# Performance work log

Measured on AMD Instinct MI355X. Metric: run time of the kernel, lower is better.

## Reference

```python
import jax, jax.numpy as jnp
import numpy as np

G = 4          # moe_groups
EPG = 4        # experts per group = e_num // moe_groups
E = 16         # e_num
KG = 2         # moe_max_groups
K = 2          # moe_max_k
GTP = 0.9      # moe_group_top_p
TP = 0.9       # moe_top_p
SCALE = 1.0 / float(np.sqrt(G))  # group_scale


def setup_inputs() -> dict:
    key = jax.random.key(0)
    ks = jax.random.split(key, 6)
    B, T, D, H = 2, 1024, 512, 2048  # H = 4*emb_dim per SwiGLU_FFN(emb_dim, 4*emb_dim)
    x = jax.random.normal(ks[0], (B, T, D), jnp.float32)
    Wr = jax.random.normal(ks[1], (D, G), jnp.float32) * 0.02      # group_router weight
    br = jnp.zeros((G,), jnp.float32)                               # group_router bias
    Wgate = jax.random.normal(ks[2], (G, D, EPG), jnp.float32) * 0.02  # per-group gates
    bgate = jnp.zeros((G, EPG), jnp.float32)
    W1 = jax.random.normal(ks[3], (E, D, H), jnp.float32) * 0.02   # SwiGLU gate proj
    W3 = jax.random.normal(ks[4], (E, D, H), jnp.float32) * 0.02   # SwiGLU up proj
    W2 = jax.random.normal(ks[5], (E, H, D), jnp.float32) * 0.02   # SwiGLU down proj
    return {"x": x, "Wr": Wr, "br": br, "Wgate": Wgate, "bgate": bgate,
            "W1": W1, "W3": W3, "W2": W2}


def _routing_weights(xf, Wr, br, Wgate, bgate):
    # Returns combined per-(token, expert) weight (N, E): group_renorm * expert_renorm * SCALE.
    N = xf.shape[0]
    # ---- group-level top-p routing ----
    gp = jax.nn.softmax(xf @ Wr + br, axis=-1)                      # (N, G)
    order = jnp.argsort(-gp, axis=-1)
    sp_k = jnp.take_along_axis(gp, order, axis=-1)[:, :KG]          # top-KG probs, descending
    idx_k = order[:, :KG]
    act = jnp.cumsum(sp_k, axis=-1) <= GTP
    act = act.at[:, 0].set(True)                                    # always keep best group
    mp = sp_k * act
    rn = mp / (jnp.sum(mp, axis=-1, keepdims=True) + 1e-9)
    w_group = jnp.zeros((N, G), xf.dtype).at[jnp.arange(N)[:, None], idx_k].set(rn)
    # ---- expert-level top-p routing within each group ----
    ep = jax.nn.softmax(jnp.einsum('nd,gde->nge', xf, Wgate) + bgate, axis=-1)  # (N, G, EPG)
    eorder = jnp.argsort(-ep, axis=-1)
    esp = jnp.take_along_axis(ep, eorder, axis=-1)[:, :, :K]
    eidx = eorder[:, :, :K]
    eact = jnp.cumsum(esp, axis=-1) <= TP
    eact = eact.at[:, :, 0].set(True)                               # always keep best expert
    emp = esp * eact
    ern = emp / (jnp.sum(emp, axis=-1, keepdims=True) + 1e-9)
    w_exp = jnp.zeros((N, G, EPG), xf.dtype).at[
        jnp.arange(N)[:, None, None], jnp.arange(G)[None, :, None], eidx].set(ern)
    return (w_group[:, :, None] * w_exp * SCALE).reshape(N, E)      # (N, E)


def reference(x, Wr, br, Wgate, bgate, W1, W3, W2):
    B, T, D = x.shape
    xf = x.reshape(-1, D)                                           # (N, D)
    tw = _routing_weights(xf, Wr, br, Wgate, bgate)                 # (N, E)
    out = jnp.zeros_like(xf)
    for e in range(E):  # fixed structural loop over experts
        h = jax.nn.silu(xf @ W1[e]) * (xf @ W3[e])                  # SwiGLU hidden (N, H)
        out = out + tw[:, e:e + 1] * (h @ W2[e])
    return out.reshape(B, T, D)
```

## Files before the change

### kernel.cpp

```cpp
#include <hip/hip_runtime.h>
#include <math.h>

typedef unsigned short u16;
typedef unsigned int   u32;
typedef short s16x8 __attribute__((ext_vector_type(8)));
typedef float f32x4 __attribute__((ext_vector_type(4)));

#define N_TOK 2048
#define DIM   512
#define HID   2048
#define NE    16
#define NG    4
#define EPG   4
#define MAXT  2048

#define BM 64
#define BN 128
#define BK 64

#define WS_CNT    0
#define WS_OFF    128
#define WS_TOKIDX 256
#define WS_TW     (WS_TOKIDX + NE*MAXT*4)
#define WS_XB     (WS_TW + N_TOK*NE*4)
#define WS_HBUF   (WS_XB + (size_t)N_TOK*DIM*2)
#define WS_W1T    (WS_HBUF + (size_t)8192*HID*2)
#define WS_W3T    (WS_W1T + (size_t)NE*HID*DIM*2)
#define WS_W2T    (WS_W3T + (size_t)NE*HID*DIM*2)
#define WS_SLOT   (WS_W2T + (size_t)NE*DIM*HID*2)
#define WS_BUF2   WS_W1T

__device__ __forceinline__ int* ws_i32(void* ws, size_t off) { return (int*)((char*)ws + off); }

__device__ __forceinline__ u16 f2b(float f) {
    union { float f; u32 i; } v; v.f = f;
    u32 b = v.i;
    u32 r = b + 0x7FFFu + ((b >> 16) & 1u);
    return (u16)(r >> 16);
}

__device__ __forceinline__ void gl_lds16(const u16* g, u16* l) {
    __builtin_amdgcn_global_load_lds((const __attribute__((address_space(1))) void*)g,
                                     (__attribute__((address_space(3))) void*)l, 16, 0, 0);
}

__global__ __launch_bounds__(1024) void prep_kernel(
    const float* __restrict__ x, const float* __restrict__ Wr, const float* __restrict__ br,
    const float* __restrict__ Wgate, const float* __restrict__ bgate,
    const float* __restrict__ W1, const float* __restrict__ W3, void* ws)
{
    __shared__ u16 T[2][128*128];
    int tid = threadIdx.x;
    int bid = blockIdx.x;

    if (bid < 128) {
        int t = bid * 16 + (tid >> 6);
        int lane = tid & 63;

        float xl[8];
        {
            const float4* xr = (const float4*)(x + (size_t)t*DIM + lane*8);
            float4 a = xr[0], b = xr[1];
            xl[0]=a.x; xl[1]=a.y; xl[2]=a.z; xl[3]=a.w;
            xl[4]=b.x; xl[5]=b.y; xl[6]=b.z; xl[7]=b.w;
        }
        {
            union { u16 h[8]; uint4 q; } pk;
            #pragma unroll
            for (int i = 0; i < 8; i++) pk.h[i] = f2b(xl[i]);
            u16* xb = (u16*)((char*)ws + WS_XB);
            *(uint4*)(xb + (size_t)t*DIM + lane*8) = pk.q;
        }

        float gl[NG] = {0.f,0.f,0.f,0.f};
        float el[NE];
        #pragma unroll
        for (int e = 0; e < NE; e++) el[e] = 0.f;

        {
            const float4* Wr4 = (const float4*)Wr;
            #pragma unroll
            for (int c = 0; c < 8; c++) {
                float4 w = Wr4[lane*8 + c];
                gl[0] += xl[c]*w.x; gl[1] += xl[c]*w.y;
                gl[2] += xl[c]*w.z; gl[3] += xl[c]*w.w;
            }
        }
        {
            const float4* Wg4 = (const float4*)Wgate;
            #pragma unroll
            for (int g = 0; g < NG; g++) {
                #pragma unroll
                for (int c = 0; c < 8; c++) {
                    float4 w = Wg4[(size_t)g*DIM + lane*8 + c];
                    el[g*4+0] += xl[c]*w.x; el[g*4+1] += xl[c]*w.y;
                    el[g*4+2] += xl[c]*w.z; el[g*4+3] += xl[c]*w.w;
                }
            }
        }

        #pragma unroll
        for (int g = 0; g < NG; g++)
            #pragma unroll
            for (int s = 32; s; s >>= 1) gl[g] += __shfl_xor(gl[g], s);
        #pragma unroll
        for (int e = 0; e < NE; e++)
            #pragma unroll
            for (int s = 32; s; s >>= 1) el[e] += __shfl_xor(el[e], s);

        if (lane != 0) return;

        float gp[NG];
        float mx = -1e30f;
        #pragma unroll
        for (int g = 0; g < NG; g++) { gl[g] += br[g]; mx = fmaxf(mx, gl[g]); }
        float sum = 0.f;
        #pragma unroll
        for (int g = 0; g < NG; g++) { gp[g] = expf(gl[g] - mx); sum += gp[g]; }
        #pragma unroll
        for (int g = 0; g < NG; g++) gp[g] /= sum;

        int i0 = 0;
        #pragma unroll
        for (int g = 1; g < NG; g++) if (gp[g] > gp[i0]) i0 = g;
        int i1 = -1;
        #pragma unroll
        for (int g = 0; g < NG; g++) { if (g == i0) continue; if (i1 < 0 || gp[g] > gp[i1]) i1 = g; }

        bool act1 = (gp[i0] + gp[i1]) <= 0.9f;
        float mp0 = gp[i0], mp1 = act1 ? gp[i1] : 0.f;
        float inv = 1.f / (mp0 + mp1 + 1e-9f);
        float wg[NG] = {0.f,0.f,0.f,0.f};
        wg[i0] = mp0 * inv;
        wg[i1] = mp1 * inv;

        float tw[NE];
        #pragma unroll
        for (int g = 0; g < NG; g++) {
            float ep[EPG];
            float emx = -1e30f;
            #pragma unroll
            for (int j = 0; j < EPG; j++) {
                float v = el[g*4 + j] + bgate[g*4 + j];
                ep[j] = v; emx = fmaxf(emx, v);
            }
            float es = 0.f;
            #pragma unroll
            for (int j = 0; j < EPG; j++) { ep[j] = expf(ep[j] - emx); es += ep[j]; }
            #pragma unroll
            for (int j = 0; j < EPG; j++) ep[j] /= es;

            int j0 = 0;
            #pragma unroll
            for (int j = 1; j < EPG; j++) if (ep[j] > ep[j0]) j0 = j;
            int j1 = -1;
            #pragma unroll
            for (int j = 0; j < EPG; j++) { if (j == j0) continue; if (j1 < 0 || ep[j] > ep[j1]) j1 = j; }

            bool ea1 = (ep[j0] + ep[j1]) <= 0.9f;
            float e0 = ep[j0], e1 = ea1 ? ep[j1] : 0.f;
            float einv = 1.f / (e0 + e1 + 1e-9f);
            float we[EPG] = {0.f,0.f,0.f,0.f};
            we[j0] = e0 * einv;
            we[j1] = e1 * einv;
            #pragma unroll
            for (int j = 0; j < EPG; j++) tw[g*4 + j] = wg[g] * we[j] * 0.5f;
        }

        float* twT = (float*)((char*)ws + WS_TW);
        #pragma unroll
        for (int e = 0; e < NE; e++) twT[(size_t)e*N_TOK + t] = tw[e];
        return;
    }

    int bx = bid - 128;
    int j = tid & 31, i0 = tid >> 5;
    int tg0 = bx * 4;

    const float* src; u16* dst; int k0, n0;
    float4 v0, v1, v2, v3;

    auto setup = [&](int tg) {
        int mat = tg >> 10, e = (tg >> 6) & 15, w = tg & 63;
        const float* s  = mat ? W3 : W1;
        u16* d = (u16*)((char*)ws + (mat ? WS_W3T : WS_W1T));
        k0 = (w & 3) << 7; n0 = (w >> 2) << 7;
        src = s + (size_t)e*DIM*HID + (size_t)(k0 + 4*i0)*HID + n0 + 4*j;
        dst = d + (size_t)e*HID*DIM;
    };
    auto issue_loads = [&]() {
        v0 = *(const float4*)(src);
        v1 = *(const float4*)(src + HID);
        v2 = *(const float4*)(src + 2*HID);
        v3 = *(const float4*)(src + 3*HID);
    };

    setup(tg0);
    issue_loads();

    for (int it = 0; it < 4; ++it) {
        u16* dstc = dst; int k0c = k0, n0c = n0;
        u16* Tb = &T[it & 1][0];

        int pc = 4 * (i0 ^ ((j & 15) << 1));
        union { u16 h[4]; uint2 q; } p;
        p.h[0]=f2b(v0.x); p.h[1]=f2b(v1.x); p.h[2]=f2b(v2.x); p.h[3]=f2b(v3.x);
        *(uint2*)(&Tb[(4*j+0)*128 + pc]) = p.q;
        p.h[0]=f2b(v0.y); p.h[1]=f2b(v1.y); p.h[2]=f2b(v2.y); p.h[3]=f2b(v3.y);
        *(uint2*)(&Tb[(4*j+1)*128 + pc]) = p.q;
        p.h[0]=f2b(v0.z); p.h[1]=f2b(v1.z); p.h[2]=f2b(v2.z); p.h[3]=f2b(v3.z);
        *(uint2*)(&Tb[(4*j+2)*128 + pc]) = p.q;
        p.h[0]=f2b(v0.w); p.h[1]=f2b(v1.w); p.h[2]=f2b(v2.w); p.h[3]=f2b(v3.w);
        *(uint2*)(&Tb[(4*j+3)*128 + pc]) = p.q;

        if (it + 1 < 4) { setup(tg0 + it + 1); issue_loads(); }

        asm volatile("s_waitcnt lgkmcnt(0)" ::: "memory");
        __builtin_amdgcn_s_barrier();

        #pragma unroll
        for (int ph = 0; ph < 2; ++ph) {
            int idx = tid + ph*1024;
            int nr = idx >> 4, sg = idx & 15;
            int cp = (2*sg) ^ (((nr >> 2) & 15) << 1);
            *(s16x8*)(dstc + (size_t)(n0c+nr)*DIM + k0c + sg*8) = *(const s16x8*)(&Tb[nr*128 + 4*cp]);
        }
    }
}

__global__ __launch_bounds__(1024) void expert_scan_kernel(void* ws)
{
    int tid = threadIdx.x;
    int e = tid >> 6, lane = tid & 63;
    const float* twT = (const float*)((char*)ws + WS_TW) + (size_t)e*N_TOK;
    int* tok = ws_i32(ws, WS_TOKIDX) + e*MAXT;
    __shared__ int scnt[NE];
    __shared__ int soff[NE+1];

    float v[32];
    #pragma unroll
    for (int r = 0; r < 32; r++) v[r] = twT[r*64 + lane];

    unsigned long long lanemask = (1ull << lane) - 1ull;
    int base = 0;
    #pragma unroll
    for (int r = 0; r < 32; r++) {
        bool a = v[r] > 0.f;
        unsigned long long m = __ballot(a);
        if (a) tok[base + __popcll(m & lanemask)] = r*64 + lane;
        base += __popcll(m);
    }
    if (lane == 0) scnt[e] = base;
    __syncthreads();
    if (tid == 0) {
        int* cnt = ws_i32(ws, WS_CNT);
        int* off = ws_i32(ws, WS_OFF);
        int s = 0;
        for (int i = 0; i < NE; i++) { cnt[i] = scnt[i]; off[i] = s; soff[i] = s; s += scnt[i]; }
        off[NE] = s; soff[NE] = s;
    }
    __syncthreads();

    int* slot_of = ws_i32(ws, WS_SLOT) + e*N_TOK;
    int base2 = soff[e];
    #pragma unroll
    for (int r = 0; r < 32; r++) {
        bool a = v[r] > 0.f;
        unsigned long long m = __ballot(a);
        int pre = __popcll(m & lanemask);
        slot_of[r*64 + lane] = a ? (base2 + pre) : -1;
        base2 += __popcll(m);
    }
}

__global__ __launch_bounds__(256) void gemm1_fast(const float* __restrict__ W2, void* ws)
{
    __shared__ __align__(16) u16 SM[40960];
    int z = blockIdx.z;
    int tid = threadIdx.x;

    if (z == NE) {
        u16* T2 = SM;
        u16* W2T = (u16*)((char*)ws + WS_W2T);
        int slot = blockIdx.x + 16*blockIdx.y;
        int j = tid & 31, i = tid >> 5;
        #pragma unroll 1
        for (int tt = 0; tt < 2; ++tt) {
            int tile = slot + tt*512;
            int e = tile >> 6, w = tile & 63;
            int k0 = (w & 15) << 7, n0 = (w >> 4) << 7;
            const float* s = W2 + (size_t)e*HID*DIM + (size_t)k0*DIM + n0 + 4*j;
            if (tt) __syncthreads();
            #pragma unroll
            for (int c = 0; c < 4; ++c) {
                int kb = 4*i + 32*c;
                const float* base = s + (size_t)kb*DIM;
                float4 v0 = *(const float4*)(base);
                float4 v1 = *(const float4*)(base + DIM);
                float4 v2 = *(const float4*)(base + 2*DIM);
                float4 v3 = *(const float4*)(base + 3*DIM);
                int pc = 4 * ((i + 8*c) ^ ((j & 15) << 1));
                union { u16 h[4]; uint2 q; } p;
                p.h[0]=f2b(v0.x); p.h[1]=f2b(v1.x); p.h[2]=f2b(v2.x); p.h[3]=f2b(v3.x);
                *(uint2*)(&T2[(4*j+0)*128 + pc]) = p.q;
                p.h[0]=f2b(v0.y); p.h[1]=f2b(v1.y); p.h[2]=f2b(v2.y); p.h[3]=f2b(v3.y);
                *(uint2*)(&T2[(4*j+1)*128 + pc]) = p.q;
                p.h[0]=f2b(v0.z); p.h[1]=f2b(v1.z); p.h[2]=f2b(v2.z); p.h[3]=f2b(v3.z);
                *(uint2*)(&T2[(4*j+2)*128 + pc]) = p.q;
                p.h[0]=f2b(v0.w); p.h[1]=f2b(v1.w); p.h[2]=f2b(v2.w); p.h[3]=f2b(v3.w);
                *(uint2*)(&T2[(4*j+3)*128 + pc]) = p.q;
            }
            __syncthreads();
            u16* d = W2T + (size_t)e*DIM*HID;
            #pragma unroll
            for (int ph = 0; ph < 8; ++ph) {
                int idx = tid + ph*256;
                int nr = idx >> 4, sg = idx & 15;
                int cp = (2*sg) ^ (((nr >> 2) & 15) << 1);
                *(s16x8*)(d + (size_t)(n0+nr)*HID + k0 + sg*8) = *(const s16x8*)(&T2[nr*128 + 4*cp]);
            }
        }
        return;
    }

    int e  = z;
    const int* cnt = ws_i32(ws, WS_CNT);
    int ce = cnt[e];
    int m0 = blockIdx.y * BM;
    if (m0 >= ce) return;
    int n0 = blockIdx.x * BN;

    const int* off = ws_i32(ws, WS_OFF);
    const int* tok = ws_i32(ws, WS_TOKIDX) + e*MAXT;
    const u16* xb  = (const u16*)((char*)ws + WS_XB);
    const u16* W1T = (const u16*)((char*)ws + WS_W1T) + (size_t)e*HID*DIM;
    const u16* W3T = (const u16*)((char*)ws + WS_W3T) + (size_t)e*HID*DIM;
    u16* hbuf = (u16*)((char*)ws + WS_HBUF);
    int obase = off[e] + m0;

    int wave = tid >> 6, lane = tid & 63;
    int quad = lane >> 4, l16 = lane & 15;
    int swz  = l16 & 7;
    int r8 = lane >> 3, sg = lane & 7;
    int swk = ((sg ^ r8) << 3);

    int m_a0 = m0 + wave*16 + r8;     if (m_a0 >= ce) m_a0 = ce - 1;
    int m_a1 = m0 + wave*16 + 8 + r8; if (m_a1 >= ce) m_a1 = ce - 1;
    const u16* arow0 = xb + (size_t)tok[m_a0]*DIM + swk;
    const u16* arow1 = xb + (size_t)tok[m_a1]*DIM + swk;
    const u16* b1row[4]; const u16* b3row[4];
    #pragma unroll
    for (int i = 0; i < 4; i++) {
        size_t nr = (size_t)(n0 + wave*32 + i*8 + r8)*DIM + swk;
        b1row[i] = W1T + nr;
        b3row[i] = W3T + nr;
    }

    f32x4 acc1[4][2], acc3[4][2];
    #pragma unroll
    for (int mt = 0; mt < 4; mt++)
        #pragma unroll
        for (int nt = 0; nt < 2; nt++) {
            acc1[mt][nt] = (f32x4){0.f,0.f,0.f,0.f};
            acc3[mt][nt] = (f32x4){0.f,0.f,0.f,0.f};
        }

    auto stage = [&](u16* B, int k0) {
        gl_lds16(arow0 + k0, B + (wave*16)*BK);
        gl_lds16(arow1 + k0, B + (wave*16 + 8)*BK);
        #pragma unroll
        for (int i = 0; i < 4; i++) {
            gl_lds16(b1row[i] + k0, B + 4096 + (wave*32 + i*8)*BK);
            gl_lds16(b3row[i] + k0, B + 12288 + (wave*32 + i*8)*BK);
        }
    };
    auto compute = [&](const u16* B) {
        #pragma unroll
        for (int kk = 0; kk < BK; kk += 32) {
            int jj = (kk >> 3) + quad;
            int so = ((jj ^ swz) << 3);
            s16x8 af[4];
            #pragma unroll
            for (int mt = 0; mt < 4; mt++)
                af[mt] = *(const s16x8*)(B + (mt*16 + l16)*BK + so);
            #pragma unroll
            for (int nt = 0; nt < 2; nt++) {
                int n = wave*32 + nt*16 + l16;
                s16x8 b1 = *(const s16x8*)(B + 4096 + n*BK + so);
                s16x8 b3 = *(const s16x8*)(B + 12288 + n*BK + so);
                #pragma unroll
                for (int mt = 0; mt < 4; mt++) {
                    acc1[mt][nt] = __builtin_amdgcn_mfma_f32_16x16x32_bf16(af[mt], b1, acc1[mt][nt], 0, 0, 0);
                    acc3[mt][nt] = __builtin_amdgcn_mfma_f32_16x16x32_bf16(af[mt], b3, acc3[mt][nt], 0, 0, 0);
                }
            }
        }
    };

    u16* SM0 = SM;
    u16* SM1 = SM + 20480;

    stage(SM0, 0);
    #pragma unroll 1
    for (int kt2 = 0; kt2 < 3; ++kt2) {
        int kb = kt2*2*BK;
        stage(SM1, kb + BK);
        asm volatile("s_waitcnt vmcnt(10)" ::: "memory");
        __builtin_amdgcn_s_barrier();
        compute(SM0);
        __builtin_amdgcn_s_barrier();
        stage(SM0, kb + 2*BK);
        asm volatile("s_waitcnt vmcnt(10)" ::: "memory");
        __builtin_amdgcn_s_barrier();
        compute(SM1);
        __builtin_amdgcn_s_barrier();
    }
    stage(SM1, 7*BK);
    asm volatile("s_waitcnt vmcnt(10)" ::: "memory");
    __builtin_amdgcn_s_barrier();
    compute(SM0);
    __builtin_amdgcn_s_barrier();
    asm volatile("s_waitcnt vmcnt(0)" ::: "memory");
    __builtin_amdgcn_s_barrier();
    compute(SM1);

    #pragma unroll
    for (int mt = 0; mt < 4; mt++) {
        #pragma unroll
        for (int r = 0; r < 4; r++) {
            int row = mt*16 + quad*4 + r;
            if (m0 + row < ce) {
                #pragma unroll
                for (int nt = 0; nt < 2; nt++) {
                    float a = acc1[mt][nt][r];
                    float b = acc3[mt][nt][r];
                    float h = (a / (1.f + expf(-a))) * b;
                    int col = wave*32 + nt*16 + l16;
                    hbuf[(size_t)(obase + row)*HID + n0 + col] = f2b(h);
                }
            }
        }
    }
}

__global__ __launch_bounds__(256) void gemm2_fast(void* ws)
{
    __shared__ __align__(16) u16 SM[24576];
    int e  = blockIdx.z;
    const int* cnt = ws_i32(ws, WS_CNT);
    int ce = cnt[e];
    int m0 = blockIdx.y * BM;
    if (m0 >= ce) return;
    int n0 = blockIdx.x * BN;

    const int* off = ws_i32(ws, WS_OFF);
    const int* tok = ws_i32(ws, WS_TOKIDX) + e*MAXT;
    const float* twT = (const float*)((char*)ws + WS_TW);
    const u16* hbuf = (const u16*)((char*)ws + WS_HBUF);
    const u16* W2T = (const u16*)((char*)ws + WS_W2T) + (size_t)e*DIM*HID;
    float* buf2 = (float*)((char*)ws + WS_BUF2);
    int abase = off[e] + m0;
    int total = off[NE];

    int tid = threadIdx.x;
    int wave = tid >> 6, lane = tid & 63;
    int quad = lane >> 4, l16 = lane & 15;
    int swz  = l16 & 7;
    int r8 = lane >> 3, sg = lane & 7;
    int swk = ((sg ^ r8) << 3);

    int ar0 = abase + wave*16 + r8;      if (ar0 > total - 1) ar0 = total - 1;
    int ar1 = abase + wave*16 + 8 + r8;  if (ar1 > total - 1) ar1 = total - 1;
    const u16* arow0 = hbuf + (size_t)ar0*HID + swk;
    const u16* arow1 = hbuf + (size_t)ar1*HID + swk;
    const u16* brow[4];
    #pragma unroll
    for (int i = 0; i < 4; i++)
        brow[i] = W2T + (size_t)(n0 + wave*32 + i*8 + r8)*HID + swk;

    f32x4 acc[4][2];
    #pragma unroll
    for (int mt = 0; mt < 4; mt++)
        #pragma unroll
        for (int nt = 0; nt < 2; nt++) acc[mt][nt] = (f32x4){0.f,0.f,0.f,0.f};

    auto stage = [&](u16* B, int k0) {
        gl_lds16(arow0 + k0, B + (wave*16)*BK);
        gl_lds16(arow1 + k0, B + (wave*16 + 8)*BK);
        #pragma unroll
        for (int i = 0; i < 4; i++)
            gl_lds16(brow[i] + k0, B + 4096 + (wave*32 + i*8)*BK);
    };
    auto compute = [&](const u16* B) {
        #pragma unroll
        for (int kk = 0; kk < BK; kk += 32) {
            int jj = (kk >> 3) + quad;
            int so = ((jj ^ swz) << 3);
            s16x8 af[4];
            #pragma unroll
            for (int mt = 0; mt < 4; mt++)
                af[mt] = *(const s16x8*)(B + (mt*16 + l16)*BK + so);
            #pragma unroll
            for (int nt = 0; nt < 2; nt++) {
                int n = wave*32 + nt*16 + l16;
                s16x8 bfr = *(const s16x8*)(B + 4096 + n*BK + so);
                #pragma unroll
                for (int mt = 0; mt < 4; mt++)
                    acc[mt][nt] = __builtin_amdgcn_mfma_f32_16x16x32_bf16(af[mt], bfr, acc[mt][nt], 0, 0, 0);
            }
        }
    };

    u16* SM0 = SM;
    u16* SM1 = SM + 12288;

    stage(SM0, 0);
    #pragma unroll 1
    for (int kt2 = 0; kt2 < 15; ++kt2) {
        int kb = kt2*2*BK;
        stage(SM1, kb + BK);
        asm volatile("s_waitcnt vmcnt(6)" ::: "memory");
        __builtin_amdgcn_s_barrier();
        compute(SM0);
        __builtin_amdgcn_s_barrier();
        stage(SM0, kb + 2*BK);
        asm volatile("s_waitcnt vmcnt(6)" ::: "memory");
        __builtin_amdgcn_s_barrier();
        compute(SM1);
        __builtin_amdgcn_s_barrier();
    }
    stage(SM1, 31*BK);
    asm volatile("s_waitcnt vmcnt(6)" ::: "memory");
    __builtin_amdgcn_s_barrier();
    compute(SM0);
    __builtin_amdgcn_s_barrier();
    asm volatile("s_waitcnt vmcnt(0)" ::: "memory");
    __builtin_amdgcn_s_barrier();
    compute(SM1);

    #pragma unroll
    for (int mt = 0; mt < 4; mt++) {
        #pragma unroll
        for (int r = 0; r < 4; r++) {
            int row = mt*16 + quad*4 + r;
            if (m0 + row < ce) {
                int t = tok[m0 + row];
                float s = twT[(size_t)e*N_TOK + t];
                #pragma unroll
                for (int nt = 0; nt < 2; nt++) {
                    int col = wave*32 + nt*16 + l16;
                    buf2[(size_t)(abase + row)*DIM + n0 + col] = acc[mt][nt][r] * s;
                }
            }
        }
    }
}

__global__ __launch_bounds__(128) void gather_kernel(void* ws, float* __restrict__ out)
{
    int t = blockIdx.x;
    int tid = threadIdx.x;
    const int* slot_of = ws_i32(ws, WS_SLOT);
    const float* buf2 = (const float*)((char*)ws + WS_BUF2);

    int d = tid * 4;
    float4 acc = {0.f, 0.f, 0.f, 0.f};
    #pragma unroll
    for (int e = 0; e < NE; e++) {
        int s = slot_of[e*N_TOK + t];
        if (s >= 0) {
            float4 v = *(const float4*)(buf2 + (size_t)s*DIM + d);
            acc.x += v.x; acc.y += v.y; acc.z += v.z; acc.w += v.w;
        }
    }
    *(float4*)(out + (size_t)t*DIM + d) = acc;
}

extern "C" void kernel_launch(void* const* d_in, const int* in_sizes, int n_in,
                              void* d_out, int out_size, void* d_ws, size_t ws_size,
                              hipStream_t stream)
{
    const float* x     = (const float*)d_in[0];
    const float* Wr    = (const float*)d_in[1];
    const float* br    = (const float*)d_in[2];
    const float* Wgate = (const float*)d_in[3];
    const float* bgate = (const float*)d_in[4];
    const float* W1    = (const float*)d_in[5];
    const float* W3    = (const float*)d_in[6];
    const float* W2    = (const float*)d_in[7];
    float* out = (float*)d_out;

    prep_kernel<<<640, 1024, 0, stream>>>(x, Wr, br, Wgate, bgate, W1, W3, d_ws);
    expert_scan_kernel<<<1, 1024, 0, stream>>>(d_ws);
    gemm1_fast<<<dim3(HID/BN, N_TOK/BM, NE + 1), 256, 0, stream>>>(W2, d_ws);
    gemm2_fast<<<dim3(DIM/BN, N_TOK/BM, NE), 256, 0, stream>>>(d_ws);
    gather_kernel<<<N_TOK, 128, 0, stream>>>(d_ws, out);
}
```

Before: 323.3 us.

## Double M tile to 128 with 8-wave 2x4 warp layout in both expert GEMMs

Raises the token tile from 64 to 128 rows and doubles the block to 512 threads, arranging the eight waves as a 2x4 grid so each weight tile loaded into LDS is reused by twice as many tokens. Staging loads are redistributed across the waves and the vmcnt waits are adjusted to match. The W2 transpose path in gemm1 is reworked for 512 threads and the grid halves in the M dimension. The aim is to cut weight traffic per FLOP; in exchange, LDS per block grows and blocks are fewer, and experts with few tokens waste more padded rows.

```diff
diff --git a/kernel.cpp b/kernel.cpp
--- a/kernel.cpp
+++ b/kernel.cpp
@@ -14,7 +14,7 @@
 #define EPG   4
 #define MAXT  2048
 
-#define BM 64
+#define BM 128
 #define BN 128
 #define BK 64
 
@@ -273,9 +273,9 @@
     }
 }
 
-__global__ __launch_bounds__(256) void gemm1_fast(const float* __restrict__ W2, void* ws)
+__global__ __launch_bounds__(512) void gemm1_fast(const float* __restrict__ W2, void* ws)
 {
-    __shared__ __align__(16) u16 SM[40960];
+    __shared__ __align__(16) u16 SM[49152];
     int z = blockIdx.z;
     int tid = threadIdx.x;
 
@@ -285,21 +285,21 @@
         int slot = blockIdx.x + 16*blockIdx.y;
         int j = tid & 31, i = tid >> 5;
         #pragma unroll 1
-        for (int tt = 0; tt < 2; ++tt) {
-            int tile = slot + tt*512;
+        for (int tt = 0; tt < 4; ++tt) {
+            int tile = slot + tt*256;
             int e = tile >> 6, w = tile & 63;
             int k0 = (w & 15) << 7, n0 = (w >> 4) << 7;
             const float* s = W2 + (size_t)e*HID*DIM + (size_t)k0*DIM + n0 + 4*j;
             if (tt) __syncthreads();
             #pragma unroll
-            for (int c = 0; c < 4; ++c) {
-                int kb = 4*i + 32*c;
+            for (int c = 0; c < 2; ++c) {
+                int kb = 4*i + 64*c;
                 const float* base = s + (size_t)kb*DIM;
                 float4 v0 = *(const float4*)(base);
                 float4 v1 = *(const float4*)(base + DIM);
                 float4 v2 = *(const float4*)(base + 2*DIM);
                 float4 v3 = *(const float4*)(base + 3*DIM);
-                int pc = 4 * ((i + 8*c) ^ ((j & 15) << 1));
+                int pc = 4 * ((i + 16*c) ^ ((j & 15) << 1));
                 union { u16 h[4]; uint2 q; } p;
                 p.h[0]=f2b(v0.x); p.h[1]=f2b(v1.x); p.h[2]=f2b(v2.x); p.h[3]=f2b(v3.x);
                 *(uint2*)(&T2[(4*j+0)*128 + pc]) = p.q;
@@ -313,8 +313,8 @@
             __syncthreads();
             u16* d = W2T + (size_t)e*DIM*HID;
             #pragma unroll
-            for (int ph = 0; ph < 8; ++ph) {
-                int idx = tid + ph*256;
+            for (int ph = 0; ph < 4; ++ph) {
+                int idx = tid + ph*512;
                 int nr = idx >> 4, sg = idx & 15;
                 int cp = (2*sg) ^ (((nr >> 2) & 15) << 1);
                 *(s16x8*)(d + (size_t)(n0+nr)*HID + k0 + sg*8) = *(const s16x8*)(&T2[nr*128 + 4*cp]);
@@ -339,6 +339,7 @@
     int obase = off[e] + m0;
 
     int wave = tid >> 6, lane = tid & 63;
+    int wr = wave >> 2, wc = wave & 3;
     int quad = lane >> 4, l16 = lane & 15;
     int swz  = l16 & 7;
     int r8 = lane >> 3, sg = lane & 7;
@@ -348,13 +349,10 @@
     int m_a1 = m0 + wave*16 + 8 + r8; if (m_a1 >= ce) m_a1 = ce - 1;
     const u16* arow0 = xb + (size_t)tok[m_a0]*DIM + swk;
     const u16* arow1 = xb + (size_t)tok[m_a1]*DIM + swk;
-    const u16* b1row[4]; const u16* b3row[4];
-    #pragma unroll
-    for (int i = 0; i < 4; i++) {
-        size_t nr = (size_t)(n0 + wave*32 + i*8 + r8)*DIM + swk;
-        b1row[i] = W1T + nr;
-        b3row[i] = W3T + nr;
-    }
+    const u16* b1r0 = W1T + (size_t)(n0 + wave*16 + r8)*DIM + swk;
+    const u16* b1r1 = W1T + (size_t)(n0 + wave*16 + 8 + r8)*DIM + swk;
+    const u16* b3r0 = W3T + (size_t)(n0 + wave*16 + r8)*DIM + swk;
+    const u16* b3r1 = W3T + (size_t)(n0 + wave*16 + 8 + r8)*DIM + swk;
 
     f32x4 acc1[4][2], acc3[4][2];
     #pragma unroll
@@ -368,11 +366,10 @@
     auto stage = [&](u16* B, int k0) {
         gl_lds16(arow0 + k0, B + (wave*16)*BK);
         gl_lds16(arow1 + k0, B + (wave*16 + 8)*BK);
-        #pragma unroll
-        for (int i = 0; i < 4; i++) {
-            gl_lds16(b1row[i] + k0, B + 4096 + (wave*32 + i*8)*BK);
-            gl_lds16(b3row[i] + k0, B + 12288 + (wave*32 + i*8)*BK);
-        }
+        gl_lds16(b1r0 + k0, B + 8192 + (wave*16)*BK);
+        gl_lds16(b1r1 + k0, B + 8192 + (wave*16 + 8)*BK);
+        gl_lds16(b3r0 + k0, B + 16384 + (wave*16)*BK);
+        gl_lds16(b3r1 + k0, B + 16384 + (wave*16 + 8)*BK);
     };
     auto compute = [&](const u16* B) {
         #pragma unroll
@@ -382,12 +379,12 @@
             s16x8 af[4];
             #pragma unroll
             for (int mt = 0; mt < 4; mt++)
-                af[mt] = *(const s16x8*)(B + (mt*16 + l16)*BK + so);
+                af[mt] = *(const s16x8*)(B + (wr*64 + mt*16 + l16)*BK + so);
             #pragma unroll
             for (int nt = 0; nt < 2; nt++) {
-                int n = wave*32 + nt*16 + l16;
-                s16x8 b1 = *(const s16x8*)(B + 4096 + n*BK + so);
-                s16x8 b3 = *(const s16x8*)(B + 12288 + n*BK + so);
+                int n = wc*32 + nt*16 + l16;
+                s16x8 b1 = *(const s16x8*)(B + 8192 + n*BK + so);
+                s16x8 b3 = *(const s16x8*)(B + 16384 + n*BK + so);
                 #pragma unroll
                 for (int mt = 0; mt < 4; mt++) {
                     acc1[mt][nt] = __builtin_amdgcn_mfma_f32_16x16x32_bf16(af[mt], b1, acc1[mt][nt], 0, 0, 0);
@@ -398,25 +395,25 @@
     };
 
     u16* SM0 = SM;
-    u16* SM1 = SM + 20480;
+    u16* SM1 = SM + 24576;
 
     stage(SM0, 0);
     #pragma unroll 1
     for (int kt2 = 0; kt2 < 3; ++kt2) {
         int kb = kt2*2*BK;
         stage(SM1, kb + BK);
-        asm volatile("s_waitcnt vmcnt(10)" ::: "memory");
+        asm volatile("s_waitcnt vmcnt(6)" ::: "memory");
         __builtin_amdgcn_s_barrier();
         compute(SM0);
         __builtin_amdgcn_s_barrier();
         stage(SM0, kb + 2*BK);
-        asm volatile("s_waitcnt vmcnt(10)" ::: "memory");
+        asm volatile("s_waitcnt vmcnt(6)" ::: "memory");
         __builtin_amdgcn_s_barrier();
         compute(SM1);
         __builtin_amdgcn_s_barrier();
     }
     stage(SM1, 7*BK);
-    asm volatile("s_waitcnt vmcnt(10)" ::: "memory");
+    asm volatile("s_waitcnt vmcnt(6)" ::: "memory");
     __builtin_amdgcn_s_barrier();
     compute(SM0);
     __builtin_amdgcn_s_barrier();
@@ -428,14 +425,14 @@
     for (int mt = 0; mt < 4; mt++) {
         #pragma unroll
         for (int r = 0; r < 4; r++) {
-            int row = mt*16 + quad*4 + r;
+            int row = wr*64 + mt*16 + quad*4 + r;
             if (m0 + row < ce) {
                 #pragma unroll
                 for (int nt = 0; nt < 2; nt++) {
                     float a = acc1[mt][nt][r];
                     float b = acc3[mt][nt][r];
                     float h = (a / (1.f + expf(-a))) * b;
-                    int col = wave*32 + nt*16 + l16;
+                    int col = wc*32 + nt*16 + l16;
                     hbuf[(size_t)(obase + row)*HID + n0 + col] = f2b(h);
                 }
             }
@@ -443,9 +440,9 @@
     }
 }
 
-__global__ __launch_bounds__(256) void gemm2_fast(void* ws)
+__global__ __launch_bounds__(512) void gemm2_fast(void* ws)
 {
-    __shared__ __align__(16) u16 SM[24576];
+    __shared__ __align__(16) u16 SM[32768];
     int e  = blockIdx.z;
     const int* cnt = ws_i32(ws, WS_CNT);
     int ce = cnt[e];
@@ -464,6 +461,7 @@
 
     int tid = threadIdx.x;
     int wave = tid >> 6, lane = tid & 63;
+    int wr = wave >> 2, wc = wave & 3;
     int quad = lane >> 4, l16 = lane & 15;
     int swz  = l16 & 7;
     int r8 = lane >> 3, sg = lane & 7;
@@ -473,10 +471,8 @@
     int ar1 = abase + wave*16 + 8 + r8;  if (ar1 > total - 1) ar1 = total - 1;
     const u16* arow0 = hbuf + (size_t)ar0*HID + swk;
     const u16* arow1 = hbuf + (size_t)ar1*HID + swk;
-    const u16* brow[4];
-    #pragma unroll
-    for (int i = 0; i < 4; i++)
-        brow[i] = W2T + (size_t)(n0 + wave*32 + i*8 + r8)*HID + swk;
+    const u16* br0 = W2T + (size_t)(n0 + wave*16 + r8)*HID + swk;
+    const u16* br1 = W2T + (size_t)(n0 + wave*16 + 8 + r8)*HID + swk;
 
     f32x4 acc[4][2];
     #pragma unroll
@@ -487,9 +483,8 @@
     auto stage = [&](u16* B, int k0) {
         gl_lds16(arow0 + k0, B + (wave*16)*BK);
         gl_lds16(arow1 + k0, B + (wave*16 + 8)*BK);
-        #pragma unroll
-        for (int i = 0; i < 4; i++)
-            gl_lds16(brow[i] + k0, B + 4096 + (wave*32 + i*8)*BK);
+        gl_lds16(br0 + k0, B + 8192 + (wave*16)*BK);
+        gl_lds16(br1 + k0, B + 8192 + (wave*16 + 8)*BK);
     };
     auto compute = [&](const u16* B) {
         #pragma unroll
@@ -499,11 +494,11 @@
             s16x8 af[4];
             #pragma unroll
             for (int mt = 0; mt < 4; mt++)
-                af[mt] = *(const s16x8*)(B + (mt*16 + l16)*BK + so);
+                af[mt] = *(const s16x8*)(B + (wr*64 + mt*16 + l16)*BK + so);
             #pragma unroll
             for (int nt = 0; nt < 2; nt++) {
-                int n = wave*32 + nt*16 + l16;
-                s16x8 bfr = *(const s16x8*)(B + 4096 + n*BK + so);
+                int n = wc*32 + nt*16 + l16;
+                s16x8 bfr = *(const s16x8*)(B + 8192 + n*BK + so);
                 #pragma unroll
                 for (int mt = 0; mt < 4; mt++)
                     acc[mt][nt] = __builtin_amdgcn_mfma_f32_16x16x32_bf16(af[mt], bfr, acc[mt][nt], 0, 0, 0);
@@ -512,25 +507,25 @@
     };
 
     u16* SM0 = SM;
-    u16* SM1 = SM + 12288;
+    u16* SM1 = SM + 16384;
 
     stage(SM0, 0);
     #pragma unroll 1
     for (int kt2 = 0; kt2 < 15; ++kt2) {
         int kb = kt2*2*BK;
         stage(SM1, kb + BK);
-        asm volatile("s_waitcnt vmcnt(6)" ::: "memory");
+        asm volatile("s_waitcnt vmcnt(4)" ::: "memory");
         __builtin_amdgcn_s_barrier();
         compute(SM0);
         __builtin_amdgcn_s_barrier();
         stage(SM0, kb + 2*BK);
-        asm volatile("s_waitcnt vmcnt(6)" ::: "memory");
+        asm volatile("s_waitcnt vmcnt(4)" ::: "memory");
         __builtin_amdgcn_s_barrier();
         compute(SM1);
         __builtin_amdgcn_s_barrier();
     }
     stage(SM1, 31*BK);
-    asm volatile("s_waitcnt vmcnt(6)" ::: "memory");
+    asm volatile("s_waitcnt vmcnt(4)" ::: "memory");
     __builtin_amdgcn_s_barrier();
     compute(SM0);
     __builtin_amdgcn_s_barrier();
@@ -542,13 +537,13 @@
     for (int mt = 0; mt < 4; mt++) {
         #pragma unroll
         for (int r = 0; r < 4; r++) {
-            int row = mt*16 + quad*4 + r;
+            int row = wr*64 + mt*16 + quad*4 + r;
             if (m0 + row < ce) {
                 int t = tok[m0 + row];
                 float s = twT[(size_t)e*N_TOK + t];
                 #pragma unroll
                 for (int nt = 0; nt < 2; nt++) {
-                    int col = wave*32 + nt*16 + l16;
+                    int col = wc*32 + nt*16 + l16;
                     buf2[(size_t)(abase + row)*DIM + n0 + col] = acc[mt][nt][r] * s;
                 }
             }
@@ -592,7 +587,7 @@
 
     prep_kernel<<<640, 1024, 0, stream>>>(x, Wr, br, Wgate, bgate, W1, W3, d_ws);
     expert_scan_kernel<<<1, 1024, 0, stream>>>(d_ws);
-    gemm1_fast<<<dim3(HID/BN, N_TOK/BM, NE + 1), 256, 0, stream>>>(W2, d_ws);
-    gemm2_fast<<<dim3(DIM/BN, N_TOK/BM, NE), 256, 0, stream>>>(d_ws);
+    gemm1_fast<<<dim3(HID/BN, N_TOK/BM, NE + 1), 512, 0, stream>>>(W2, d_ws);
+    gemm2_fast<<<dim3(DIM/BN, N_TOK/BM, NE), 512, 0, stream>>>(d_ws);
     gather_kernel<<<N_TOK, 128, 0, stream>>>(d_ws, out);
 }
```

Result: no change. 322.3 us (-0.3%).
